# Kernel optimization log

Measured on AMD Instinct MI355X. Metric: run time of the kernel, lower is better.

Reference implementation:

```python
import jax, jax.numpy as jnp
import numpy as np

D_MODEL = 1024
N_HEADS = 16
HEAD_DIM = D_MODEL // N_HEADS
BATCH = 2
SEQ = 2048


def setup_inputs() -> dict:
    key = jax.random.key(0)
    ks = jax.random.split(key, 9)
    s = 1.0 / np.sqrt(D_MODEL)
    inp = {
        "x": jax.random.normal(ks[0], (BATCH, SEQ, D_MODEL), dtype=jnp.float32),
        "Wq": jax.random.uniform(ks[1], (D_MODEL, D_MODEL), jnp.float32, -s, s),
        "bq": jax.random.uniform(ks[2], (D_MODEL,), jnp.float32, -s, s),
        "Wk": jax.random.uniform(ks[3], (D_MODEL, D_MODEL), jnp.float32, -s, s),
        "bk": jax.random.uniform(ks[4], (D_MODEL,), jnp.float32, -s, s),
        "Wv": jax.random.uniform(ks[5], (D_MODEL, D_MODEL), jnp.float32, -s, s),
        "bv": jax.random.uniform(ks[6], (D_MODEL,), jnp.float32, -s, s),
        "Wo": jax.random.uniform(ks[7], (D_MODEL, D_MODEL), jnp.float32, -s, s),
        "bo": jax.random.uniform(ks[8], (D_MODEL,), jnp.float32, -s, s),
    }
    return inp


def reference(x, Wq, bq, Wk, bk, Wv, bv, Wo, bo):
    B, S, _ = x.shape
    # projections -> [B, H, S, Dh]
    def proj(W, b):
        y = jnp.einsum('bsd,df->bsf', x, W) + b
        return y.reshape(B, S, N_HEADS, HEAD_DIM).transpose(0, 2, 1, 3)
    q = proj(Wq, bq)
    k = proj(Wk, bk)
    v = proj(Wv, bv)
    scores = jnp.einsum('bhqd,bhkd->bhqk', q, k) / jnp.sqrt(jnp.float32(HEAD_DIM))
    mask = jnp.tril(jnp.ones((S, S), dtype=bool))  # [S, S] causal mask
    scores = jnp.where(mask, scores, -jnp.inf)
    weights = jax.nn.softmax(scores, axis=-1)
    h = jnp.einsum('bhqk,bhkd->bhqd', weights, v)
    h = h.transpose(0, 2, 1, 3).reshape(B, S, N_HEADS * HEAD_DIM)
    return jnp.einsum('bsd,df->bsf', h, Wo) + bo
```

## Files before the change

kernel.cpp:

```cpp
#include <hip/hip_runtime.h>
#include <hip/hip_bf16.h>
#include <cmath>

#define D_MODEL 1024
#define NHEADS 16
#define HDIM 64
#define BATCH 2
#define SEQ 2048
#define MROWS (BATCH*SEQ)
#define KDIM 1024

typedef unsigned short ushort_t;
typedef unsigned int uint32;
typedef __attribute__((ext_vector_type(8))) short short8;
typedef __attribute__((ext_vector_type(4))) short short4b;
typedef __attribute__((ext_vector_type(4))) float floatx4;

#define QSCALE 0.1803368801111204f
#define EXP2F(x) __builtin_amdgcn_exp2f(x)

__device__ __forceinline__ ushort_t f2bf(float x) {
    union { float f; uint32 u; } v; v.f = x;
    uint32 r = v.u + 0x7FFFu + ((v.u >> 16) & 1u);
    return (ushort_t)(r >> 16);
}

__device__ __forceinline__ uint32 pkbf(float a, float b) {
    union { __hip_bfloat162 h2; uint32 u; } v;
    v.h2 = __float22bfloat162_rn(make_float2(a, b));
    return v.u;
}

__device__ __forceinline__ void glds16(const void* g, void* l) {
    __builtin_amdgcn_global_load_lds(
        (const __attribute__((address_space(1))) void*)g,
        (__attribute__((address_space(3))) void*)l, 16, 0, 0);
}

__global__ __launch_bounds__(256)
void cvt_all(const float* __restrict__ x, const float* __restrict__ W0,
             const float* __restrict__ W1, const float* __restrict__ W2,
             const float* __restrict__ W3, ushort_t* __restrict__ xb,
             ushort_t* __restrict__ WtQKV, ushort_t* __restrict__ WtO)
{
    const int z = blockIdx.z;
    if (z == 4) {
        size_t idx = ((size_t)blockIdx.y * 32 + blockIdx.x) * 256 + threadIdx.x;
        #pragma unroll
        for (int l = 0; l < 4; ++l) {
            size_t i = ((size_t)l * 262144 + idx) * 4;
            float4 v = *(const float4*)(x + i);
            uint2 o;
            o.x = pkbf(v.x, v.y);
            o.y = pkbf(v.z, v.w);
            *(uint2*)(xb + i) = o;
        }
        return;
    }
    __shared__ float tl[32][33];
    const float* W = (z == 0) ? W0 : (z == 1) ? W1 : (z == 2) ? W2 : W3;
    ushort_t* out = (z < 3) ? (WtQKV + (size_t)z * D_MODEL * KDIM) : WtO;
    const int k0 = blockIdx.x * 32, n0 = blockIdx.y * 32;
    const int tx = threadIdx.x & 31, ty = threadIdx.x >> 5;
    #pragma unroll
    for (int i = 0; i < 4; ++i)
        tl[ty + i * 8][tx] = W[(size_t)(k0 + ty + i * 8) * D_MODEL + n0 + tx];
    __syncthreads();
    #pragma unroll
    for (int i = 0; i < 4; ++i)
        out[(size_t)(n0 + ty + i * 8) * KDIM + k0 + tx] = f2bf(tl[tx][ty + i * 8]);
}

__global__ __launch_bounds__(128, 2)
void gemm_qkv(const ushort_t* __restrict__ A, const ushort_t* __restrict__ Bt,
              const float* __restrict__ b0, const float* __restrict__ b1,
              const float* __restrict__ b2, ushort_t* __restrict__ Qb,
              ushort_t* __restrict__ Kb, ushort_t* __restrict__ Vb)
{
    __shared__ ushort_t As[128 * 64];
    __shared__ ushort_t Bs[128 * 64];

    const int tid = threadIdx.x;
    const int w = tid >> 6, lane = tid & 63;
    const int quad = lane >> 4, col = lane & 15;
    const int m0 = blockIdx.y * 128, n0 = blockIdx.x * 128;

    floatx4 zero = {0.f, 0.f, 0.f, 0.f};
    floatx4 acc[4][8];
    #pragma unroll
    for (int i = 0; i < 4; ++i)
        #pragma unroll
        for (int j = 0; j < 8; ++j) acc[i][j] = zero;

    #pragma unroll 1
    for (int k0 = 0; k0 < KDIM; k0 += 64) {
        #pragma unroll
        for (int i = 0; i < 8; ++i) {
            int c = i * 128 + tid;
            int row = c >> 3;
            int kc = (c & 7) ^ (row & 7);
            glds16(A  + (size_t)(m0 + row) * KDIM + k0 + kc * 8, As + (i * 128 + w * 64) * 8);
            glds16(Bt + (size_t)(n0 + row) * KDIM + k0 + kc * 8, Bs + (i * 128 + w * 64) * 8);
        }
        __syncthreads();
        #pragma unroll
        for (int ks = 0; ks < 2; ++ks) {
            short8 af[4], bfr[8];
            const int kc = ks * 4 + quad;
            #pragma unroll
            for (int mt = 0; mt < 4; ++mt) {
                int r = w * 64 + mt * 16 + col;
                af[mt] = *(const short8*)(As + ((size_t)r * 8 + (kc ^ (r & 7))) * 8);
            }
            #pragma unroll
            for (int nt = 0; nt < 8; ++nt) {
                int r = nt * 16 + col;
                bfr[nt] = *(const short8*)(Bs + ((size_t)r * 8 + (kc ^ (r & 7))) * 8);
            }
            #pragma unroll
            for (int mt = 0; mt < 4; ++mt)
                #pragma unroll
                for (int nt = 0; nt < 8; ++nt)
                    acc[mt][nt] = __builtin_amdgcn_mfma_f32_16x16x32_bf16(
                        af[mt], bfr[nt], acc[mt][nt], 0, 0, 0);
        }
        __syncthreads();
    }

    const int which = n0 >> 10;
    const float* bp = (which == 0) ? b0 : (which == 1) ? b1 : b2;
    if (which < 2) {
        ushort_t* outp = (which == 0) ? Qb : Kb;
        const float scl = (which == 0) ? QSCALE : 1.0f;
        #pragma unroll
        for (int mt = 0; mt < 4; ++mt)
            #pragma unroll
            for (int nt = 0; nt < 8; ++nt) {
                int nn = (n0 + nt * 16 + col) & 1023;
                float bb = bp[nn];
                int h = nn >> 6, d = nn & 63;
                #pragma unroll
                for (int r = 0; r < 4; ++r) {
                    int m = m0 + w * 64 + mt * 16 + quad * 4 + r;
                    int b = m >> 11, s = m & 2047;
                    outp[((size_t)(b * NHEADS + h) * SEQ + s) * HDIM + d] =
                        f2bf((acc[mt][nt][r] + bb) * scl);
                }
            }
    } else {
        #pragma unroll
        for (int mt = 0; mt < 4; ++mt)
            #pragma unroll
            for (int nt = 0; nt < 8; ++nt) {
                int nn = (n0 + nt * 16 + col) & 1023;
                float bb = bp[nn];
                int h = nn >> 6, d = nn & 63;
                int mb = m0 + w * 64 + mt * 16 + quad * 4;
                int b = mb >> 11, s = mb & 2047;
                uint2 pw;
                pw.x = pkbf(acc[mt][nt][0] + bb, acc[mt][nt][1] + bb);
                pw.y = pkbf(acc[mt][nt][2] + bb, acc[mt][nt][3] + bb);
                *(uint2*)(Vb + ((size_t)(b * NHEADS + h) * HDIM + d) * SEQ + s) = pw;
            }
    }
}

__global__ __launch_bounds__(128, 2)
void gemm_o(const ushort_t* __restrict__ A, const ushort_t* __restrict__ Bt,
            const float* __restrict__ b0, float* __restrict__ Cf)
{
    __shared__ ushort_t As[128 * 64];
    __shared__ ushort_t Bs[64 * 64];

    const int tid = threadIdx.x;
    const int w = tid >> 6, lane = tid & 63;
    const int quad = lane >> 4, col = lane & 15;
    const int m0 = blockIdx.y * 128, n0 = blockIdx.x * 64;

    floatx4 zero = {0.f, 0.f, 0.f, 0.f};
    floatx4 acc[4][4];
    #pragma unroll
    for (int i = 0; i < 4; ++i)
        #pragma unroll
        for (int j = 0; j < 4; ++j) acc[i][j] = zero;

    #pragma unroll 1
    for (int k0 = 0; k0 < KDIM; k0 += 64) {
        #pragma unroll
        for (int i = 0; i < 8; ++i) {
            int c = i * 128 + tid;
            int row = c >> 3;
            int kc = (c & 7) ^ (row & 7);
            glds16(A + (size_t)(m0 + row) * KDIM + k0 + kc * 8, As + (i * 128 + w * 64) * 8);
        }
        #pragma unroll
        for (int i = 0; i < 4; ++i) {
            int c = i * 128 + tid;
            int row = c >> 3;
            int kc = (c & 7) ^ (row & 7);
            glds16(Bt + (size_t)(n0 + row) * KDIM + k0 + kc * 8, Bs + (i * 128 + w * 64) * 8);
        }
        __syncthreads();
        #pragma unroll
        for (int ks = 0; ks < 2; ++ks) {
            short8 af[4], bfr[4];
            const int kc = ks * 4 + quad;
            #pragma unroll
            for (int mt = 0; mt < 4; ++mt) {
                int r = w * 64 + mt * 16 + col;
                af[mt] = *(const short8*)(As + ((size_t)r * 8 + (kc ^ (r & 7))) * 8);
            }
            #pragma unroll
            for (int nt = 0; nt < 4; ++nt) {
                int r = nt * 16 + col;
                bfr[nt] = *(const short8*)(Bs + ((size_t)r * 8 + (kc ^ (r & 7))) * 8);
            }
            #pragma unroll
            for (int mt = 0; mt < 4; ++mt)
                #pragma unroll
                for (int nt = 0; nt < 4; ++nt)
                    acc[mt][nt] = __builtin_amdgcn_mfma_f32_16x16x32_bf16(
                        af[mt], bfr[nt], acc[mt][nt], 0, 0, 0);
        }
        __syncthreads();
    }

    #pragma unroll
    for (int mt = 0; mt < 4; ++mt)
        #pragma unroll
        for (int nt = 0; nt < 4; ++nt) {
            int n = n0 + nt * 16 + col;
            float bb = b0[n];
            #pragma unroll
            for (int r = 0; r < 4; ++r) {
                int m = m0 + w * 64 + mt * 16 + quad * 4 + r;
                Cf[(size_t)m * D_MODEL + n] = acc[mt][nt][r] + bb;
            }
        }
}

__global__ __launch_bounds__(256)
void attn_mfma(const ushort_t* __restrict__ Q, const ushort_t* __restrict__ K,
               const ushort_t* __restrict__ Vt, ushort_t* __restrict__ H)
{
    __shared__ __align__(16) float smemf[16640];
    ushort_t* Qs  = (ushort_t*)smemf;
    ushort_t* Ksm = (ushort_t*)(smemf + 2048);
    ushort_t* Vsm = (ushort_t*)(smemf + 6144);
    float* Ored = smemf;
    float* Lred = smemf + 16384;

    const int tid = threadIdx.x;
    const int w = tid >> 6, lane = tid & 63;
    const int quad = lane >> 4, col = lane & 15;
    const int blk = blockIdx.x;
    const int bh = (blk & 7) * 4 + ((blk >> 3) & 3);
    const int pair = blk >> 5;
    const size_t base = (size_t)bh * SEQ * HDIM;
    const ushort_t* Kb = K + base;
    const ushort_t* Vb = Vt + base;
    const int b = bh >> 4, h = bh & 15;

    const int c0 = (w * 2 + 0) * 64 + lane;
    const int c1 = (w * 2 + 1) * 64 + lane;
    const int r0 = c0 >> 3, o0 = ((c0 & 7) ^ (r0 & 7)) * 8;
    const int r1 = c1 >> 3, o1 = ((c1 & 7) ^ (r1 & 7)) * 8;

    const int rk = w * 16 + col;
    const floatx4 zero = {0.f, 0.f, 0.f, 0.f};

    #pragma unroll 1
    for (int pi = 0; pi < 2; ++pi) {
        const int qt = pi ? pair : 31 - pair;
        const int q0 = qt * 64;
        const int nt = qt + 1;

        __syncthreads();
        #pragma unroll
        for (int i = 0; i < 2; ++i) {
            int c = (w * 2 + i) * 64 + lane;
            int row = c >> 3, kc = (c & 7) ^ (row & 7);
            glds16(Q + base + (size_t)(q0 + row) * HDIM + kc * 8, Qs + (w * 2 + i) * 512);
        }
        glds16(Kb + (size_t)r0 * HDIM + o0, Ksm + (w * 2 + 0) * 512);
        glds16(Kb + (size_t)r1 * HDIM + o1, Ksm + (w * 2 + 1) * 512);
        glds16(Vb + (size_t)r0 * SEQ + o0,  Vsm + (w * 2 + 0) * 512);
        glds16(Vb + (size_t)r1 * SEQ + o1,  Vsm + (w * 2 + 1) * 512);
        __syncthreads();

        short8 bq[4][2];
        #pragma unroll
        for (int qb = 0; qb < 4; ++qb)
            #pragma unroll
            for (int ks = 0; ks < 2; ++ks) {
                int rq = qb * 16 + col;
                int kc = ks * 4 + quad;
                bq[qb][ks] = *(const short8*)(Qs + ((size_t)rq * 8 + (kc ^ (rq & 7))) * 8);
            }

        floatx4 o_[4][4];
        #pragma unroll
        for (int i = 0; i < 4; ++i)
            #pragma unroll
            for (int j = 0; j < 4; ++j) o_[i][j] = zero;
        float lq[4] = {0.f, 0.f, 0.f, 0.f};

        #pragma unroll 1
        for (int t = 0; t < nt; ++t) {
            const ushort_t* Kcur = Ksm + (t & 1) * 4096;
            const ushort_t* Vcur = Vsm + (t & 1) * 4096;
            if (t + 1 < nt) {
                const int k0n = (t + 1) * 64;
                ushort_t* Kn = Ksm + ((t + 1) & 1) * 4096;
                ushort_t* Vn = Vsm + ((t + 1) & 1) * 4096;
                glds16(Kb + (size_t)(k0n + r0) * HDIM + o0, Kn + (w * 2 + 0) * 512);
                glds16(Kb + (size_t)(k0n + r1) * HDIM + o1, Kn + (w * 2 + 1) * 512);
                glds16(Vb + (size_t)r0 * SEQ + k0n + o0,    Vn + (w * 2 + 0) * 512);
                glds16(Vb + (size_t)r1 * SEQ + k0n + o1,    Vn + (w * 2 + 1) * 512);
            }

            floatx4 sc[4];
            #pragma unroll
            for (int qb = 0; qb < 4; ++qb) sc[qb] = zero;
            __builtin_amdgcn_s_setprio(1);
            #pragma unroll
            for (int ks = 0; ks < 2; ++ks) {
                const int kc = ks * 4 + quad;
                short8 ak = *(const short8*)(Kcur + ((size_t)rk * 8 + (kc ^ (rk & 7))) * 8);
                #pragma unroll
                for (int qb = 0; qb < 4; ++qb)
                    sc[qb] = __builtin_amdgcn_mfma_f32_16x16x32_bf16(
                        ak, bq[qb][ks], sc[qb], 0, 0, 0);
            }
            __builtin_amdgcn_s_setprio(0);

            if (t == nt - 1) {
                #pragma unroll
                for (int qb = 0; qb < 4; ++qb)
                    #pragma unroll
                    for (int r = 0; r < 4; ++r)
                        if (w * 16 + quad * 4 + r > qb * 16 + col) sc[qb][r] = -INFINITY;
            }

            short4b bp[4];
            #pragma unroll
            for (int qb = 0; qb < 4; ++qb) {
                float p0 = EXP2F(sc[qb][0]);
                float p1 = EXP2F(sc[qb][1]);
                float p2 = EXP2F(sc[qb][2]);
                float p3 = EXP2F(sc[qb][3]);
                lq[qb] += (p0 + p1) + (p2 + p3);
                union { uint2 u; short4b s; } pv;
                pv.u.x = pkbf(p0, p1);
                pv.u.y = pkbf(p2, p3);
                bp[qb] = pv.s;
            }

            const int cc = 2 * w + (quad >> 1);
            const int sub = (quad & 1) * 4;
            __builtin_amdgcn_s_setprio(1);
            #pragma unroll
            for (int db = 0; db < 4; ++db) {
                int rv = db * 16 + col;
                short4b av = *(const short4b*)(Vcur + ((size_t)rv * 8 + (cc ^ (rv & 7))) * 8 + sub);
                #pragma unroll
                for (int qb = 0; qb < 4; ++qb)
                    o_[db][qb] = __builtin_amdgcn_mfma_f32_16x16x16bf16_1k(
                        av, bp[qb], o_[db][qb], 0, 0, 0);
            }
            __builtin_amdgcn_s_setprio(0);

            __syncthreads();
        }

        #pragma unroll
        for (int qb = 0; qb < 4; ++qb) {
            lq[qb] += __shfl_xor(lq[qb], 16);
            lq[qb] += __shfl_xor(lq[qb], 32);
        }
        if (quad == 0) {
            #pragma unroll
            for (int qb = 0; qb < 4; ++qb) Lred[w * 64 + qb * 16 + col] = lq[qb];
        }
        {
            float* myreg = Ored + w * 4096;
            #pragma unroll
            for (int db = 0; db < 4; ++db)
                #pragma unroll
                for (int qb = 0; qb < 4; ++qb) {
                    int q = qb * 16 + col;
                    int swch = (db * 4 + quad) ^ col;
                    *(floatx4*)(myreg + q * 64 + swch * 4) = o_[db][qb];
                }
        }
        __syncthreads();

        {
            const int qloc = w * 16 + (lane >> 2);
            float lsum = Lred[qloc] + Lred[64 + qloc] + Lred[128 + qloc] + Lred[192 + qloc];
            float linv = 1.f / lsum;
            const int dc0 = (lane & 3) * 4;
            floatx4 acc[4];
            #pragma unroll
            for (int j = 0; j < 4; ++j) {
                int swch = (dc0 + j) ^ (qloc & 15);
                const float* p = Ored + (size_t)qloc * 64 + swch * 4;
                floatx4 a = *(const floatx4*)p;
                a += *(const floatx4*)(p + 4096);
                a += *(const floatx4*)(p + 8192);
                a += *(const floatx4*)(p + 12288);
                acc[j] = a;
            }
            const size_t rowb = ((size_t)(b * SEQ + q0 + qloc)) * D_MODEL + h * HDIM + dc0 * 4;
            uint4 u0, u1;
            u0.x = pkbf(acc[0][0] * linv, acc[0][1] * linv);
            u0.y = pkbf(acc[0][2] * linv, acc[0][3] * linv);
            u0.z = pkbf(acc[1][0] * linv, acc[1][1] * linv);
            u0.w = pkbf(acc[1][2] * linv, acc[1][3] * linv);
            u1.x = pkbf(acc[2][0] * linv, acc[2][1] * linv);
            u1.y = pkbf(acc[2][2] * linv, acc[2][3] * linv);
            u1.z = pkbf(acc[3][0] * linv, acc[3][1] * linv);
            u1.w = pkbf(acc[3][2] * linv, acc[3][3] * linv);
            *(uint4*)(H + rowb) = u0;
            *(uint4*)(H + rowb + 8) = u1;
        }
    }
}

extern "C" void kernel_launch(void* const* d_in, const int* in_sizes, int n_in,
                              void* d_out, int out_size, void* d_ws, size_t ws_size,
                              hipStream_t stream)
{
    (void)in_sizes; (void)n_in; (void)out_size; (void)ws_size;
    const float* x  = (const float*)d_in[0];
    const float* Wq = (const float*)d_in[1];
    const float* bq = (const float*)d_in[2];
    const float* Wk = (const float*)d_in[3];
    const float* bk = (const float*)d_in[4];
    const float* Wv = (const float*)d_in[5];
    const float* bv = (const float*)d_in[6];
    const float* Wo = (const float*)d_in[7];
    const float* bo = (const float*)d_in[8];

    const size_t E = (size_t)MROWS * D_MODEL;
    ushort_t* xb    = (ushort_t*)d_ws;
    ushort_t* WtQKV = xb + E;
    ushort_t* WtO   = WtQKV + 3 * (size_t)D_MODEL * KDIM;
    ushort_t* Qb    = WtO + (size_t)D_MODEL * KDIM;
    ushort_t* Kb    = Qb + E;
    ushort_t* Vb    = Kb + E;
    ushort_t* Hb    = Vb + E;

    cvt_all<<<dim3(32, 32, 5), 256, 0, stream>>>(x, Wq, Wk, Wv, Wo, xb, WtQKV, WtO);
    gemm_qkv<<<dim3(24, 32), 128, 0, stream>>>(xb, WtQKV, bq, bk, bv, Qb, Kb, Vb);
    attn_mfma<<<dim3(512), 256, 0, stream>>>(Qb, Kb, Vb, Hb);
    gemm_o<<<dim3(16, 32), 128, 0, stream>>>(Hb, WtO, bo, (float*)d_out);
}
```

Baseline: 179.3 us.

## Triple-buffer K/V and software-pipeline next tile's QK^T with current softmax/PV

The attention kernel moves from double to triple LDS buffering of K and V tiles, prefetching two tiles ahead. The QK^T MFMAs for tile t+1 now run between the exp/pack step and the PV MFMAs of tile t. The goal is to overlap the transcendental work with matrix work and hide global-to-LDS latency better. In exchange it uses more LDS and more registers for the second score accumulator, which could lower occupancy.

```diff
diff --git a/kernel.cpp b/kernel.cpp
--- a/kernel.cpp
+++ b/kernel.cpp
@@ -245,8 +245,8 @@
 {
     __shared__ __align__(16) float smemf[16640];
     ushort_t* Qs  = (ushort_t*)smemf;
-    ushort_t* Ksm = (ushort_t*)(smemf + 2048);
-    ushort_t* Vsm = (ushort_t*)(smemf + 6144);
+    ushort_t* Ksb = (ushort_t*)(smemf + 2048);
+    ushort_t* Vsb = (ushort_t*)(smemf + 8192);
     float* Ored = smemf;
     float* Lred = smemf + 16384;
 
@@ -282,10 +282,16 @@
             int row = c >> 3, kc = (c & 7) ^ (row & 7);
             glds16(Q + base + (size_t)(q0 + row) * HDIM + kc * 8, Qs + (w * 2 + i) * 512);
         }
-        glds16(Kb + (size_t)r0 * HDIM + o0, Ksm + (w * 2 + 0) * 512);
-        glds16(Kb + (size_t)r1 * HDIM + o1, Ksm + (w * 2 + 1) * 512);
-        glds16(Vb + (size_t)r0 * SEQ + o0,  Vsm + (w * 2 + 0) * 512);
-        glds16(Vb + (size_t)r1 * SEQ + o1,  Vsm + (w * 2 + 1) * 512);
+        glds16(Kb + (size_t)r0 * HDIM + o0, Ksb + (w * 2 + 0) * 512);
+        glds16(Kb + (size_t)r1 * HDIM + o1, Ksb + (w * 2 + 1) * 512);
+        glds16(Vb + (size_t)r0 * SEQ + o0,  Vsb + (w * 2 + 0) * 512);
+        glds16(Vb + (size_t)r1 * SEQ + o1,  Vsb + (w * 2 + 1) * 512);
+        if (nt > 1) {
+            glds16(Kb + (size_t)(64 + r0) * HDIM + o0, Ksb + 4096 + (w * 2 + 0) * 512);
+            glds16(Kb + (size_t)(64 + r1) * HDIM + o1, Ksb + 4096 + (w * 2 + 1) * 512);
+            glds16(Vb + (size_t)r0 * SEQ + 64 + o0,    Vsb + 4096 + (w * 2 + 0) * 512);
+            glds16(Vb + (size_t)r1 * SEQ + 64 + o1,    Vsb + 4096 + (w * 2 + 1) * 512);
+        }
         __syncthreads();
 
         short8 bq[4][2];
@@ -305,50 +311,50 @@
             for (int j = 0; j < 4; ++j) o_[i][j] = zero;
         float lq[4] = {0.f, 0.f, 0.f, 0.f};
 
+        ushort_t* Kcur = Ksb;            ushort_t* Vcur = Vsb;
+        ushort_t* Knxt = Ksb + 4096;     ushort_t* Vnxt = Vsb + 4096;
+        ushort_t* Kstg = Ksb + 8192;     ushort_t* Vstg = Vsb + 8192;
+
+        floatx4 scA[4];
+        #pragma unroll
+        for (int qb = 0; qb < 4; ++qb) scA[qb] = zero;
+        __builtin_amdgcn_s_setprio(1);
+        #pragma unroll
+        for (int ks = 0; ks < 2; ++ks) {
+            const int kc = ks * 4 + quad;
+            short8 ak = *(const short8*)(Kcur + ((size_t)rk * 8 + (kc ^ (rk & 7))) * 8);
+            #pragma unroll
+            for (int qb = 0; qb < 4; ++qb)
+                scA[qb] = __builtin_amdgcn_mfma_f32_16x16x32_bf16(
+                    ak, bq[qb][ks], scA[qb], 0, 0, 0);
+        }
+        __builtin_amdgcn_s_setprio(0);
+
         #pragma unroll 1
         for (int t = 0; t < nt; ++t) {
-            const ushort_t* Kcur = Ksm + (t & 1) * 4096;
-            const ushort_t* Vcur = Vsm + (t & 1) * 4096;
-            if (t + 1 < nt) {
-                const int k0n = (t + 1) * 64;
-                ushort_t* Kn = Ksm + ((t + 1) & 1) * 4096;
-                ushort_t* Vn = Vsm + ((t + 1) & 1) * 4096;
-                glds16(Kb + (size_t)(k0n + r0) * HDIM + o0, Kn + (w * 2 + 0) * 512);
-                glds16(Kb + (size_t)(k0n + r1) * HDIM + o1, Kn + (w * 2 + 1) * 512);
-                glds16(Vb + (size_t)r0 * SEQ + k0n + o0,    Vn + (w * 2 + 0) * 512);
-                glds16(Vb + (size_t)r1 * SEQ + k0n + o1,    Vn + (w * 2 + 1) * 512);
-            }
-
-            floatx4 sc[4];
-            #pragma unroll
-            for (int qb = 0; qb < 4; ++qb) sc[qb] = zero;
-            __builtin_amdgcn_s_setprio(1);
-            #pragma unroll
-            for (int ks = 0; ks < 2; ++ks) {
-                const int kc = ks * 4 + quad;
-                short8 ak = *(const short8*)(Kcur + ((size_t)rk * 8 + (kc ^ (rk & 7))) * 8);
-                #pragma unroll
-                for (int qb = 0; qb < 4; ++qb)
-                    sc[qb] = __builtin_amdgcn_mfma_f32_16x16x32_bf16(
-                        ak, bq[qb][ks], sc[qb], 0, 0, 0);
-            }
-            __builtin_amdgcn_s_setprio(0);
+            if (t + 2 < nt) {
+                const int k0n = (t + 2) * 64;
+                glds16(Kb + (size_t)(k0n + r0) * HDIM + o0, Kstg + (w * 2 + 0) * 512);
+                glds16(Kb + (size_t)(k0n + r1) * HDIM + o1, Kstg + (w * 2 + 1) * 512);
+                glds16(Vb + (size_t)r0 * SEQ + k0n + o0,    Vstg + (w * 2 + 0) * 512);
+                glds16(Vb + (size_t)r1 * SEQ + k0n + o1,    Vstg + (w * 2 + 1) * 512);
+            }
 
             if (t == nt - 1) {
                 #pragma unroll
                 for (int qb = 0; qb < 4; ++qb)
                     #pragma unroll
                     for (int r = 0; r < 4; ++r)
-                        if (w * 16 + quad * 4 + r > qb * 16 + col) sc[qb][r] = -INFINITY;
+                        if (w * 16 + quad * 4 + r > qb * 16 + col) scA[qb][r] = -INFINITY;
             }
 
             short4b bp[4];
             #pragma unroll
             for (int qb = 0; qb < 4; ++qb) {
-                float p0 = EXP2F(sc[qb][0]);
-                float p1 = EXP2F(sc[qb][1]);
-                float p2 = EXP2F(sc[qb][2]);
-                float p3 = EXP2F(sc[qb][3]);
+                float p0 = EXP2F(scA[qb][0]);
+                float p1 = EXP2F(scA[qb][1]);
+                float p2 = EXP2F(scA[qb][2]);
+                float p3 = EXP2F(scA[qb][3]);
                 lq[qb] += (p0 + p1) + (p2 + p3);
                 union { uint2 u; short4b s; } pv;
                 pv.u.x = pkbf(p0, p1);
@@ -356,6 +362,23 @@
                 bp[qb] = pv.s;
             }
 
+            floatx4 scB[4];
+            if (t + 1 < nt) {
+                #pragma unroll
+                for (int qb = 0; qb < 4; ++qb) scB[qb] = zero;
+                __builtin_amdgcn_s_setprio(1);
+                #pragma unroll
+                for (int ks = 0; ks < 2; ++ks) {
+                    const int kc = ks * 4 + quad;
+                    short8 ak = *(const short8*)(Knxt + ((size_t)rk * 8 + (kc ^ (rk & 7))) * 8);
+                    #pragma unroll
+                    for (int qb = 0; qb < 4; ++qb)
+                        scB[qb] = __builtin_amdgcn_mfma_f32_16x16x32_bf16(
+                            ak, bq[qb][ks], scB[qb], 0, 0, 0);
+                }
+                __builtin_amdgcn_s_setprio(0);
+            }
+
             const int cc = 2 * w + (quad >> 1);
             const int sub = (quad & 1) * 4;
             __builtin_amdgcn_s_setprio(1);
@@ -371,6 +394,13 @@
             __builtin_amdgcn_s_setprio(0);
 
             __syncthreads();
+
+            ushort_t* tk = Kcur; Kcur = Knxt; Knxt = Kstg; Kstg = tk;
+            ushort_t* tv = Vcur; Vcur = Vnxt; Vnxt = Vstg; Vstg = tv;
+            if (t + 1 < nt) {
+                #pragma unroll
+                for (int qb = 0; qb < 4; ++qb) scA[qb] = scB[qb];
+            }
         }
 
         #pragma unroll
```

Result: faster. 175.4 us (-2.2%).
